# Kernel optimization log

Measured on AMD Instinct MI355X. Metric: run time of the kernel, lower is better.

## Reference

```python
import jax, jax.numpy as jnp
import numpy as np
from jax import lax

B, T = 512, 2048
VOCAB, E, H, OUT = 50257, 8, 2, 128


def _lstm_layer(x_seq, W_ih, W_hh, b):
    """x_seq: [B,T,D]; W_ih: [4H,D]; W_hh: [4H,H]; b: [4H] (b_ih+b_hh)."""
    Bn = x_seq.shape[0]
    gates_x = jnp.einsum('btd,gd->btg', x_seq, W_ih) + b  # [B,T,4H]
    h0 = jnp.zeros((Bn, H), x_seq.dtype)
    c0 = jnp.zeros((Bn, H), x_seq.dtype)

    def step(carry, gx):
        h, c = carry
        g = gx + h @ W_hh.T  # [B,4H]
        i, f, gg, o = jnp.split(g, 4, axis=-1)
        c = jax.nn.sigmoid(f) * c + jax.nn.sigmoid(i) * jnp.tanh(gg)
        h = jax.nn.sigmoid(o) * jnp.tanh(c)
        return (h, c), h

    (hT, cT), ys = lax.scan(step, (h0, c0), gates_x.transpose(1, 0, 2))
    return ys.transpose(1, 0, 2), hT, cT  # [B,T,H], [B,H], [B,H]


def setup_inputs() -> dict:
    key = jax.random.key(0)
    ks = jax.random.split(key, 10)
    s = lambda fan: 1.0 / np.sqrt(fan)
    u = lambda k, shape, a: jax.random.uniform(k, shape, jnp.float32, -a, a)
    x = jax.random.randint(ks[0], (B, T), 0, VOCAB)
    emb = jax.random.normal(ks[1], (VOCAB, E), jnp.float32)
    a = s(H)
    W_ih0 = u(ks[2], (4 * H, E), a)
    W_hh0 = u(ks[3], (4 * H, H), a)
    b0 = u(ks[4], (4 * H,), a) * 2.0  # b_ih + b_hh combined
    W_ih1 = u(ks[5], (4 * H, H), a)
    W_hh1 = u(ks[6], (4 * H, H), a)
    b1 = u(ks[7], (4 * H,), a) * 2.0
    W_fc = u(ks[8], (OUT, H), s(H))
    b_fc = u(ks[9], (OUT,), s(H))
    return {"x": x, "emb": emb, "W_ih0": W_ih0, "W_hh0": W_hh0, "b0": b0,
            "W_ih1": W_ih1, "W_hh1": W_hh1, "b1": b1, "W_fc": W_fc, "b_fc": b_fc}


def reference(x, emb, W_ih0, W_hh0, b0, W_ih1, W_hh1, b1, W_fc, b_fc):
    embedded = emb[x]  # [B,T,E]
    y0, h0, c0 = _lstm_layer(embedded, W_ih0, W_hh0, b0)
    y1, h1, c1 = _lstm_layer(y0, W_ih1, W_hh1, b1)
    h_n = jnp.stack([h0, h1], axis=0)  # [n_layer,B,H]
    c_n = jnp.stack([c0, c1], axis=0)
    out = y1.reshape(-1, H) @ W_fc.T + b_fc  # [B*T, OUT]
    return out, h_n, c_n
```

## Files before the change

kernel.cpp:

```cpp
#include <hip/hip_runtime.h>

#define VOCAB 50257
#define NB 512
#define NT 2048
#define NOUT 128
#define CHUNK 32
#define L2E 1.4426950408889634f

#define QP_XOR1 0xB1
#define QP_PAIR 0xA0
#define QP_CROSS 0x0A

template<int CTRL>
__device__ __forceinline__ float qp(float v){
    return __int_as_float(__builtin_amdgcn_update_dpp(0, __float_as_int(v), CTRL, 0xF, 0xF, true));
}

__global__ __launch_bounds__(256) void build_table(const float* __restrict__ emb,
                                                   const float* __restrict__ Wih0,
                                                   const float* __restrict__ b0,
                                                   float* __restrict__ tab){
    int v = blockIdx.x*256 + threadIdx.x;
    if (v >= VOCAB) return;
    const float4* ep = (const float4*)(emb + (size_t)v*8);
    float4 e0 = ep[0], e1 = ep[1];
    float e[8] = {e0.x,e0.y,e0.z,e0.w,e1.x,e1.y,e1.z,e1.w};
    const int perm[8] = {0,2,4,6,1,3,5,7};
    float o[8];
#pragma unroll
    for (int p=0;p<8;p++){
        int rj = perm[p];
        float s = b0[rj];
#pragma unroll
        for (int d=0;d<8;d++) s = fmaf(e[d], Wih0[rj*8+d], s);
        o[p] = s * ((rj==4||rj==5) ? 2.0f*L2E : -L2E);
    }
    float4* tp = (float4*)(tab + (size_t)v*8);
    tp[0] = make_float4(o[0],o[1],o[2],o[3]);
    tp[1] = make_float4(o[4],o[5],o[6],o[7]);
}

__global__ __launch_bounds__(256) void expand_gates(const int* __restrict__ x,
                                                    const float* __restrict__ tab,
                                                    float4* __restrict__ gx){
    int gid = blockIdx.x*256 + threadIdx.x;
    int t = gid >> 9;
    int b = gid & (NB-1);
    int tok = x[(size_t)b*NT + t];
    const float4* tp = (const float4*)tab + (size_t)tok*2;
    float4 v0 = tp[0], v1 = tp[1];
    gx[(size_t)gid*2]   = v0;
    gx[(size_t)gid*2+1] = v1;
}

#define GATE_COMBINE(x0, x1) { \
    float ex0 = __builtin_amdgcn_exp2f(x0); \
    float ex1 = __builtin_amdgcn_exp2f(x1); \
    float r0 = __builtin_amdgcn_rcpf(1.0f+ex0); \
    float r1 = __builtin_amdgcn_rcpf(1.0f+ex1); \
    float v0 = fmaf(B0, r0, A0); \
    float u0 = qp<QP_XOR1>(v0); \
    float u1 = qp<QP_XOR1>(r1); \
    c = fmaf(r1, c, v0*u0); \
    float e2c = __builtin_amdgcn_exp2f(2.0f*L2E*c); \
    float th = fmaf(-2.0f, __builtin_amdgcn_rcpf(1.0f+e2c), 1.0f); \
    float hh = u1*th; \
    hs = qp<QP_PAIR>(hh); \
    ho = qp<QP_CROSS>(hh); }

__global__ __launch_bounds__(128) void lstm_pipe(const float2* __restrict__ gx,
                                                 const float* __restrict__ Whh0,
                                                 const float* __restrict__ Wih1,
                                                 const float* __restrict__ Whh1,
                                                 const float* __restrict__ b1,
                                                 float* __restrict__ y1out,
                                                 float* __restrict__ tail){
    __shared__ float h0buf[2][CHUNK][16][2];
    const int tid  = threadIdx.x;
    const int wv   = tid >> 6;
    const int lane = tid & 63;
    const int l    = lane & 3;
    const int lrow = lane >> 2;
    const int row  = blockIdx.x*16 + lrow;
    const int e    = l >> 1;
    const int rj0  = (l&1)*4 + e;
    const int rj1  = rj0 + 2;
    const float s0 = (l&1) ? 2.0f*L2E : -L2E;
    const float s1 = -L2E;
    const float A0 = (l&1) ? 1.0f : 0.0f;
    const float B0 = (l&1) ? -2.0f : 1.0f;

    const float wS0 = Whh0[rj0*2+e]*s0,  wO0 = Whh0[rj0*2+(e^1)]*s0;
    const float wS1 = Whh0[rj1*2+e]*s1,  wO1 = Whh0[rj1*2+(e^1)]*s1;
    const float wi00 = Wih1[rj0*2+0]*s0, wi01 = Wih1[rj0*2+1]*s0;
    const float wi10 = Wih1[rj1*2+0]*s1, wi11 = Wih1[rj1*2+1]*s1;
    const float whS0 = Whh1[rj0*2+e]*s0, whO0 = Whh1[rj0*2+(e^1)]*s0;
    const float whS1 = Whh1[rj1*2+e]*s1, whO1 = Whh1[rj1*2+(e^1)]*s1;
    const float bb0  = b1[rj0]*s0,       bb1  = b1[rj1]*s1;

    float hs=0.f, ho=0.f, c=0.f;
    const size_t ST = (size_t)NB*4;
    const float2* __restrict__ gp = gx + (size_t)row*4 + l;
    float2 f0,f1,f2,f3,f4,f5,f6,f7;
    if (wv==0){
        f0=gp[0*ST]; f1=gp[1*ST]; f2=gp[2*ST]; f3=gp[3*ST];
        f4=gp[4*ST]; f5=gp[5*ST]; f6=gp[6*ST]; f7=gp[7*ST];
    }

    for (int cidx=0; cidx<=NT/CHUNK; ++cidx){
        if (wv==0){
            if (cidx < NT/CHUNK){
                const int buf = cidx & 1;
                const int base = cidx*CHUNK;
#define PSTEP(F, SS) { \
    float2 nf = gp[(size_t)(base+(SS)+8)*ST];  \
    float x0 = fmaf(wS0,hs, fmaf(wO0,ho, F.x)); \
    float x1 = fmaf(wS1,hs, fmaf(wO1,ho, F.y)); \
    GATE_COMBINE(x0, x1) \
    h0buf[buf][SS][lrow][e] = hs; \
    F = nf; }
                for (int s=0; s<CHUNK; s+=8){
                    PSTEP(f0,s+0) PSTEP(f1,s+1) PSTEP(f2,s+2) PSTEP(f3,s+3)
                    PSTEP(f4,s+4) PSTEP(f5,s+5) PSTEP(f6,s+6) PSTEP(f7,s+7)
                }
#undef PSTEP
            }
        } else {
            if (cidx >= 1){
                const int buf = (cidx-1) & 1;
                const int base = (cidx-1)*CHUNK;
#pragma unroll 8
                for (int s=0; s<CHUNK; ++s){
                    const float2 h0v = *(const float2*)&h0buf[buf][s][lrow][0];
                    float x0 = fmaf(whS0,hs, fmaf(whO0,ho, fmaf(wi00,h0v.x, fmaf(wi01,h0v.y, bb0))));
                    float x1 = fmaf(whS1,hs, fmaf(whO1,ho, fmaf(wi10,h0v.x, fmaf(wi11,h0v.y, bb1))));
                    GATE_COMBINE(x0, x1)
                    y1out[((size_t)(base+s)*NB + row)*2 + e] = hs;
                }
            }
        }
        __syncthreads();
    }
    const float cs = qp<QP_PAIR>(c);
    if (wv==0){
        tail[row*2+e]          = hs;
        tail[2*NB*2 + row*2+e] = cs;
    } else {
        tail[NB*2 + row*2+e]   = hs;
        tail[3*NB*2 + row*2+e] = cs;
    }
}

__global__ __launch_bounds__(256) void fc_out(const float* __restrict__ y1,
                                              const float* __restrict__ Wfc,
                                              const float* __restrict__ bfc,
                                              float* __restrict__ out){
    const int tid = threadIdx.x;
    const int j4  = tid & 31;
    const int btl = tid >> 5;
    const int bt  = blockIdx.x*8 + btl;
    const int b   = bt >> 11;
    const int tt  = bt & (NT-1);
    const float2 y  = *(const float2*)(y1 + ((size_t)tt*NB + b)*2);
    const float4 wa = *(const float4*)(Wfc + j4*8);
    const float4 wb = *(const float4*)(Wfc + j4*8+4);
    const float4 bbv= *(const float4*)(bfc + j4*4);
    float4 o;
    o.x = fmaf(y.x,wa.x, fmaf(y.y,wa.y, bbv.x));
    o.y = fmaf(y.x,wa.z, fmaf(y.y,wa.w, bbv.y));
    o.z = fmaf(y.x,wb.x, fmaf(y.y,wb.y, bbv.z));
    o.w = fmaf(y.x,wb.z, fmaf(y.y,wb.w, bbv.w));
    *(float4*)(out + (size_t)bt*128 + j4*4) = o;
}

extern "C" void kernel_launch(void* const* d_in, const int* in_sizes, int n_in,
                              void* d_out, int out_size, void* d_ws, size_t ws_size,
                              hipStream_t stream){
    const int*   x    = (const int*)d_in[0];
    const float* emb  = (const float*)d_in[1];
    const float* Wih0 = (const float*)d_in[2];
    const float* Whh0 = (const float*)d_in[3];
    const float* b0   = (const float*)d_in[4];
    const float* Wih1 = (const float*)d_in[5];
    const float* Whh1 = (const float*)d_in[6];
    const float* b1   = (const float*)d_in[7];
    const float* Wfc  = (const float*)d_in[8];
    const float* bfc  = (const float*)d_in[9];
    float* out  = (float*)d_out;
    float* tab  = (float*)d_ws;
    float* y1   = tab + (size_t)VOCAB*8;
    float* tail = out + (size_t)NB*NT*NOUT;
    float4* gxs = (float4*)d_out;

    build_table<<<(VOCAB+255)/256, 256, 0, stream>>>(emb, Wih0, b0, tab);
    expand_gates<<<(NB*NT)/256, 256, 0, stream>>>(x, tab, gxs);
    lstm_pipe<<<32, 128, 0, stream>>>((const float2*)gxs, Whh0, Wih1, Whh1, b1, y1, tail);
    fc_out<<<(NB*NT)/8, 256, 0, stream>>>(y1, Wfc, bfc, out);
}
```

Baseline: 297.3 us.

## Interleave two independent batch rows per lane in LSTM recurrence to hide latency

Each lane now carries two independent batch rows (A and B) through both LSTM layers, interleaving their dependent recurrence steps. The grid is halved to 16 blocks, so each wave has two chains to alternate between and can hide the serial exp/rcp/DPP latency. The cell state is also stored pre-scaled by 2*log2(e), which removes one multiply from the critical path and is undone only when the final c is written. The cost is half as many blocks, so fewer CUs are busy, plus extra register use and a shallower gate prefetch depth (4 steps instead of 8).

```diff
diff --git a/kernel.cpp b/kernel.cpp
--- a/kernel.cpp
+++ b/kernel.cpp
@@ -6,6 +6,7 @@
 #define NOUT 128
 #define CHUNK 32
 #define L2E 1.4426950408889634f
+#define INV2L2E 0.34657359027997264f
 
 #define QP_XOR1 0xB1
 #define QP_PAIR 0xA0
@@ -53,7 +54,7 @@
     gx[(size_t)gid*2+1] = v1;
 }
 
-#define GATE_COMBINE(x0, x1) { \
+#define GATE_COMBINE(x0, x1, CC, HS, HO) { \
     float ex0 = __builtin_amdgcn_exp2f(x0); \
     float ex1 = __builtin_amdgcn_exp2f(x1); \
     float r0 = __builtin_amdgcn_rcpf(1.0f+ex0); \
@@ -61,12 +62,12 @@
     float v0 = fmaf(B0, r0, A0); \
     float u0 = qp<QP_XOR1>(v0); \
     float u1 = qp<QP_XOR1>(r1); \
-    c = fmaf(r1, c, v0*u0); \
-    float e2c = __builtin_amdgcn_exp2f(2.0f*L2E*c); \
+    CC = fmaf(r1, CC, v0*u0); \
+    float e2c = __builtin_amdgcn_exp2f(CC); \
     float th = fmaf(-2.0f, __builtin_amdgcn_rcpf(1.0f+e2c), 1.0f); \
     float hh = u1*th; \
-    hs = qp<QP_PAIR>(hh); \
-    ho = qp<QP_CROSS>(hh); }
+    HS = qp<QP_PAIR>(hh); \
+    HO = qp<QP_CROSS>(hh); }
 
 __global__ __launch_bounds__(128) void lstm_pipe(const float2* __restrict__ gx,
                                                  const float* __restrict__ Whh0,
@@ -75,20 +76,21 @@
                                                  const float* __restrict__ b1,
                                                  float* __restrict__ y1out,
                                                  float* __restrict__ tail){
-    __shared__ float h0buf[2][CHUNK][16][2];
+    __shared__ float h0buf[2][CHUNK][32][2];
     const int tid  = threadIdx.x;
     const int wv   = tid >> 6;
     const int lane = tid & 63;
     const int l    = lane & 3;
-    const int lrow = lane >> 2;
-    const int row  = blockIdx.x*16 + lrow;
+    const int q    = lane >> 2;
+    const int rowA = blockIdx.x*32 + q;
+    const int rowB = rowA + 16;
     const int e    = l >> 1;
     const int rj0  = (l&1)*4 + e;
     const int rj1  = rj0 + 2;
     const float s0 = (l&1) ? 2.0f*L2E : -L2E;
     const float s1 = -L2E;
-    const float A0 = (l&1) ? 1.0f : 0.0f;
-    const float B0 = (l&1) ? -2.0f : 1.0f;
+    const float A0 = (l&1) ? 2.0f*L2E : 0.0f;
+    const float B0 = (l&1) ? -4.0f*L2E : 1.0f;
 
     const float wS0 = Whh0[rj0*2+e]*s0,  wO0 = Whh0[rj0*2+(e^1)]*s0;
     const float wS1 = Whh0[rj1*2+e]*s1,  wO1 = Whh0[rj1*2+(e^1)]*s1;
@@ -98,56 +100,71 @@
     const float whS1 = Whh1[rj1*2+e]*s1, whO1 = Whh1[rj1*2+(e^1)]*s1;
     const float bb0  = b1[rj0]*s0,       bb1  = b1[rj1]*s1;
 
-    float hs=0.f, ho=0.f, c=0.f;
+    float hsA=0.f, hoA=0.f, cA=0.f;
+    float hsB=0.f, hoB=0.f, cB=0.f;
     const size_t ST = (size_t)NB*4;
-    const float2* __restrict__ gp = gx + (size_t)row*4 + l;
-    float2 f0,f1,f2,f3,f4,f5,f6,f7;
+    const float2* __restrict__ gpA = gx + (size_t)rowA*4 + l;
+    const float2* __restrict__ gpB = gx + (size_t)rowB*4 + l;
+    float2 a0,a1,a2,a3, b0v,b1v,b2v,b3v;
     if (wv==0){
-        f0=gp[0*ST]; f1=gp[1*ST]; f2=gp[2*ST]; f3=gp[3*ST];
-        f4=gp[4*ST]; f5=gp[5*ST]; f6=gp[6*ST]; f7=gp[7*ST];
-    }
+        a0=gpA[0*ST]; a1=gpA[1*ST]; a2=gpA[2*ST]; a3=gpA[3*ST];
+        b0v=gpB[0*ST]; b1v=gpB[1*ST]; b2v=gpB[2*ST]; b3v=gpB[3*ST];
+    }
+
+#define PSTEP(F, GP, SS, BASE, BUF, CC, HS, HO, RQ) { \
+    float2 nf = GP[(size_t)((BASE)+(SS)+4)*ST];  \
+    float x0 = fmaf(wS0,HS, fmaf(wO0,HO, F.x)); \
+    float x1 = fmaf(wS1,HS, fmaf(wO1,HO, F.y)); \
+    GATE_COMBINE(x0, x1, CC, HS, HO) \
+    h0buf[BUF][SS][RQ][e] = HS; \
+    F = nf; }
+
+#define CSTEP(SS, BASE, BUF, CC, HS, HO, RQ, ROW) { \
+    const float2 h0v = *(const float2*)&h0buf[BUF][SS][RQ][0]; \
+    float x0 = fmaf(whS0,HS, fmaf(whO0,HO, fmaf(wi00,h0v.x, fmaf(wi01,h0v.y, bb0)))); \
+    float x1 = fmaf(whS1,HS, fmaf(whO1,HO, fmaf(wi10,h0v.x, fmaf(wi11,h0v.y, bb1)))); \
+    GATE_COMBINE(x0, x1, CC, HS, HO) \
+    y1out[((size_t)((BASE)+(SS))*NB + (ROW))*2 + e] = HS; }
 
     for (int cidx=0; cidx<=NT/CHUNK; ++cidx){
         if (wv==0){
             if (cidx < NT/CHUNK){
                 const int buf = cidx & 1;
                 const int base = cidx*CHUNK;
-#define PSTEP(F, SS) { \
-    float2 nf = gp[(size_t)(base+(SS)+8)*ST];  \
-    float x0 = fmaf(wS0,hs, fmaf(wO0,ho, F.x)); \
-    float x1 = fmaf(wS1,hs, fmaf(wO1,ho, F.y)); \
-    GATE_COMBINE(x0, x1) \
-    h0buf[buf][SS][lrow][e] = hs; \
-    F = nf; }
-                for (int s=0; s<CHUNK; s+=8){
-                    PSTEP(f0,s+0) PSTEP(f1,s+1) PSTEP(f2,s+2) PSTEP(f3,s+3)
-                    PSTEP(f4,s+4) PSTEP(f5,s+5) PSTEP(f6,s+6) PSTEP(f7,s+7)
+                for (int s=0; s<CHUNK; s+=4){
+                    PSTEP(a0, gpA, s+0, base, buf, cA, hsA, hoA, q)
+                    PSTEP(b0v, gpB, s+0, base, buf, cB, hsB, hoB, q+16)
+                    PSTEP(a1, gpA, s+1, base, buf, cA, hsA, hoA, q)
+                    PSTEP(b1v, gpB, s+1, base, buf, cB, hsB, hoB, q+16)
+                    PSTEP(a2, gpA, s+2, base, buf, cA, hsA, hoA, q)
+                    PSTEP(b2v, gpB, s+2, base, buf, cB, hsB, hoB, q+16)
+                    PSTEP(a3, gpA, s+3, base, buf, cA, hsA, hoA, q)
+                    PSTEP(b3v, gpB, s+3, base, buf, cB, hsB, hoB, q+16)
                 }
-#undef PSTEP
             }
         } else {
             if (cidx >= 1){
                 const int buf = (cidx-1) & 1;
                 const int base = (cidx-1)*CHUNK;
-#pragma unroll 8
+#pragma unroll 4
                 for (int s=0; s<CHUNK; ++s){
-                    const float2 h0v = *(const float2*)&h0buf[buf][s][lrow][0];
-                    float x0 = fmaf(whS0,hs, fmaf(whO0,ho, fmaf(wi00,h0v.x, fmaf(wi01,h0v.y, bb0))));
-                    float x1 = fmaf(whS1,hs, fmaf(whO1,ho, fmaf(wi10,h0v.x, fmaf(wi11,h0v.y, bb1))));
-                    GATE_COMBINE(x0, x1)
-                    y1out[((size_t)(base+s)*NB + row)*2 + e] = hs;
+                    CSTEP(s, base, buf, cA, hsA, hoA, q,    rowA)
+                    CSTEP(s, base, buf, cB, hsB, hoB, q+16, rowB)
                 }
             }
         }
         __syncthreads();
     }
-    const float cs = qp<QP_PAIR>(c);
+#undef PSTEP
+#undef CSTEP
+    const float csA = qp<QP_PAIR>(cA) * INV2L2E;
+    const float csB = qp<QP_PAIR>(cB) * INV2L2E;
     if (wv==0){
-        tail[row*2+e]          = hs;
-        tail[2*NB*2 + row*2+e] = cs;
+        tail[rowA*2+e]          = hsA;  tail[rowB*2+e]          = hsB;
+        tail[2*NB*2 + rowA*2+e] = csA;  tail[2*NB*2 + rowB*2+e] = csB;
     } else {
-        tail[NB*2 + row*2+e]   = hs;
-        tail[3*NB*2 + row*2+e] = cs;
+        tail[NB*2 + rowA*2+e]   = hsA;  tail[NB*2 + rowB*2+e]   = hsB;
+        tail[3*NB*2 + rowA*2+e] = csA;  tail[3*NB*2 + rowB*2+e] = csB;
     }
 }
 
@@ -194,6 +211,6 @@
 
     build_table<<<(VOCAB+255)/256, 256, 0, stream>>>(emb, Wih0, b0, tab);
     expand_gates<<<(NB*NT)/256, 256, 0, stream>>>(x, tab, gxs);
-    lstm_pipe<<<32, 128, 0, stream>>>((const float2*)gxs, Whh0, Wih1, Whh1, b1, y1, tail);
+    lstm_pipe<<<16, 128, 0, stream>>>((const float2*)gxs, Whh0, Wih1, Whh1, b1, y1, tail);
     fc_out<<<(NB*NT)/8, 256, 0, stream>>>(y1, Wfc, bfc, out);
 }
```

Result: slower. 415.2 us (+39.6%).

## Spread LSTM gates over 8 lanes per row and precompute layer-1 input

Applied to the files above, without the earlier changes.

Each batch row now uses 8 lanes, one gate per lane, instead of 4 lanes handling two gates each, so the grid doubles to 64 blocks. Gate values are combined through DPP broadcasts, and the cell state is kept pre-scaled by 2*log2(e) so the tanh needs no extra multiply. The layer-0 wave now computes layer 1's input projection itself and hands it through shared memory, which shortens layer 1's critical path. The cost is more DPP ops per step and twice the lanes per row.

```diff
diff --git a/kernel.cpp b/kernel.cpp
--- a/kernel.cpp
+++ b/kernel.cpp
@@ -6,14 +6,21 @@
 #define NOUT 128
 #define CHUNK 32
 #define L2E 1.4426950408889634f
-
-#define QP_XOR1 0xB1
-#define QP_PAIR 0xA0
-#define QP_CROSS 0x0A
+#define INV2L2E 0.34657359027997264f
+
+#define DPP_XOR1 0xB1
+#define DPP_B0   0x00
+#define DPP_B2   0xAA
+#define DPP_B3   0xFF
+#define DPP_HMIR 0x141
 
 template<int CTRL>
 __device__ __forceinline__ float qp(float v){
     return __int_as_float(__builtin_amdgcn_update_dpp(0, __float_as_int(v), CTRL, 0xF, 0xF, true));
+}
+
+__device__ __forceinline__ int gate_rj(int gi, int e){
+    return (gi==0) ? e : (gi==1) ? 4+e : (gi==2) ? 2+e : 6+e;
 }
 
 __global__ __launch_bounds__(256) void build_table(const float* __restrict__ emb,
@@ -25,15 +32,15 @@
     const float4* ep = (const float4*)(emb + (size_t)v*8);
     float4 e0 = ep[0], e1 = ep[1];
     float e[8] = {e0.x,e0.y,e0.z,e0.w,e1.x,e1.y,e1.z,e1.w};
-    const int perm[8] = {0,2,4,6,1,3,5,7};
     float o[8];
 #pragma unroll
-    for (int p=0;p<8;p++){
-        int rj = perm[p];
+    for (int l=0;l<8;l++){
+        int gi = l&3, el = l>>2;
+        int rj = gate_rj(gi, el);
         float s = b0[rj];
 #pragma unroll
         for (int d=0;d<8;d++) s = fmaf(e[d], Wih0[rj*8+d], s);
-        o[p] = s * ((rj==4||rj==5) ? 2.0f*L2E : -L2E);
+        o[l] = s * ((gi==1) ? 2.0f*L2E : -L2E);
     }
     float4* tp = (float4*)(tab + (size_t)v*8);
     tp[0] = make_float4(o[0],o[1],o[2],o[3]);
@@ -53,101 +60,105 @@
     gx[(size_t)gid*2+1] = v1;
 }
 
-#define GATE_COMBINE(x0, x1) { \
-    float ex0 = __builtin_amdgcn_exp2f(x0); \
-    float ex1 = __builtin_amdgcn_exp2f(x1); \
-    float r0 = __builtin_amdgcn_rcpf(1.0f+ex0); \
-    float r1 = __builtin_amdgcn_rcpf(1.0f+ex1); \
-    float v0 = fmaf(B0, r0, A0); \
-    float u0 = qp<QP_XOR1>(v0); \
-    float u1 = qp<QP_XOR1>(r1); \
-    c = fmaf(r1, c, v0*u0); \
-    float e2c = __builtin_amdgcn_exp2f(2.0f*L2E*c); \
-    float th = fmaf(-2.0f, __builtin_amdgcn_rcpf(1.0f+e2c), 1.0f); \
-    float hh = u1*th; \
-    hs = qp<QP_PAIR>(hh); \
-    ho = qp<QP_CROSS>(hh); }
-
-__global__ __launch_bounds__(128) void lstm_pipe(const float2* __restrict__ gx,
+#define GATE8(x, CC, HOwn, HOth) { \
+    float ex = __builtin_amdgcn_exp2f(x); \
+    float r  = __builtin_amdgcn_rcpf(1.0f+ex); \
+    float v  = fmaf(Bc, r, Ac); \
+    float u  = qp<DPP_XOR1>(v); \
+    float pr = v*u;                        \
+    float prb= qp<DPP_B0>(pr); \
+    float fv = qp<DPP_B2>(v); \
+    CC = fmaf(fv, CC, prb); \
+    float e2 = __builtin_amdgcn_exp2f(CC); \
+    float r2 = __builtin_amdgcn_rcpf(1.0f+e2); \
+    float th = fmaf(-2.0f, r2, 1.0f); \
+    float ov = qp<DPP_B3>(v); \
+    float hh = ov*th;                      \
+    HOwn = hh; \
+    HOth = qp<DPP_HMIR>(hh); }
+
+__global__ __launch_bounds__(128) void lstm_pipe(const float* __restrict__ gx,
                                                  const float* __restrict__ Whh0,
                                                  const float* __restrict__ Wih1,
                                                  const float* __restrict__ Whh1,
                                                  const float* __restrict__ b1,
                                                  float* __restrict__ y1out,
                                                  float* __restrict__ tail){
-    __shared__ float h0buf[2][CHUNK][16][2];
+    __shared__ float xpre[2][CHUNK][8][8];
     const int tid  = threadIdx.x;
     const int wv   = tid >> 6;
     const int lane = tid & 63;
-    const int l    = lane & 3;
-    const int lrow = lane >> 2;
-    const int row  = blockIdx.x*16 + lrow;
-    const int e    = l >> 1;
-    const int rj0  = (l&1)*4 + e;
-    const int rj1  = rj0 + 2;
-    const float s0 = (l&1) ? 2.0f*L2E : -L2E;
-    const float s1 = -L2E;
-    const float A0 = (l&1) ? 1.0f : 0.0f;
-    const float B0 = (l&1) ? -2.0f : 1.0f;
-
-    const float wS0 = Whh0[rj0*2+e]*s0,  wO0 = Whh0[rj0*2+(e^1)]*s0;
-    const float wS1 = Whh0[rj1*2+e]*s1,  wO1 = Whh0[rj1*2+(e^1)]*s1;
-    const float wi00 = Wih1[rj0*2+0]*s0, wi01 = Wih1[rj0*2+1]*s0;
-    const float wi10 = Wih1[rj1*2+0]*s1, wi11 = Wih1[rj1*2+1]*s1;
-    const float whS0 = Whh1[rj0*2+e]*s0, whO0 = Whh1[rj0*2+(e^1)]*s0;
-    const float whS1 = Whh1[rj1*2+e]*s1, whO1 = Whh1[rj1*2+(e^1)]*s1;
-    const float bb0  = b1[rj0]*s0,       bb1  = b1[rj1]*s1;
-
-    float hs=0.f, ho=0.f, c=0.f;
-    const size_t ST = (size_t)NB*4;
-    const float2* __restrict__ gp = gx + (size_t)row*4 + l;
-    float2 f0,f1,f2,f3,f4,f5,f6,f7;
-    if (wv==0){
-        f0=gp[0*ST]; f1=gp[1*ST]; f2=gp[2*ST]; f3=gp[3*ST];
-        f4=gp[4*ST]; f5=gp[5*ST]; f6=gp[6*ST]; f7=gp[7*ST];
-    }
+    const int l    = lane & 7;
+    const int q    = lane >> 3;
+    const int row  = blockIdx.x*8 + q;
+    const int gi   = l & 3;
+    const int e    = l >> 2;
+    const int rj   = gate_rj(gi, e);
+    const float s  = (gi==1) ? 2.0f*L2E : -L2E;
+    const float Ac = (gi==1) ? 2.0f*L2E : 0.0f;
+    const float Bc = (gi==1) ? -4.0f*L2E : 1.0f;
+
+    const float wOwn0 = Whh0[rj*2+e]*s,     wOth0 = Whh0[rj*2+(e^1)]*s;
+    const float wiOwn = Wih1[rj*2+e]*s,     wiOth = Wih1[rj*2+(e^1)]*s;
+    const float bb    = b1[rj]*s;
+    const float whOwn = Whh1[rj*2+e]*s,     whOth = Whh1[rj*2+(e^1)]*s;
+
+    float hOwn=0.f, hOth=0.f, c=0.f;
+    const size_t ST = (size_t)NB*8;
+    const float* __restrict__ gp = gx + (size_t)row*8 + l;
+    float a0=0.f,a1=0.f,a2=0.f,a3=0.f;
+    if (wv==0){ a0=gp[0*ST]; a1=gp[1*ST]; a2=gp[2*ST]; a3=gp[3*ST]; }
+    const bool st = (gi==0);
+
+#define PSTEP(F, SS, BASE, BUF) { \
+    float nf = gp[(size_t)((BASE)+(SS)+4)*ST];  \
+    float x = fmaf(wOwn0,hOwn, fmaf(wOth0,hOth, F)); \
+    GATE8(x, c, hOwn, hOth) \
+    float xp = fmaf(wiOwn,hOwn, fmaf(wiOth,hOth, bb)); \
+    xpre[BUF][SS][q][l] = xp; \
+    F = nf; }
+
+#define CSTEP(SS, BASE, BUF) { \
+    float xv = xpre[BUF][SS][q][l]; \
+    float x = fmaf(whOwn,hOwn, fmaf(whOth,hOth, xv)); \
+    GATE8(x, c, hOwn, hOth) \
+    if (st) y1out[((size_t)((BASE)+(SS))*NB + row)*2 + e] = hOwn; }
 
     for (int cidx=0; cidx<=NT/CHUNK; ++cidx){
         if (wv==0){
             if (cidx < NT/CHUNK){
                 const int buf = cidx & 1;
                 const int base = cidx*CHUNK;
-#define PSTEP(F, SS) { \
-    float2 nf = gp[(size_t)(base+(SS)+8)*ST];  \
-    float x0 = fmaf(wS0,hs, fmaf(wO0,ho, F.x)); \
-    float x1 = fmaf(wS1,hs, fmaf(wO1,ho, F.y)); \
-    GATE_COMBINE(x0, x1) \
-    h0buf[buf][SS][lrow][e] = hs; \
-    F = nf; }
-                for (int s=0; s<CHUNK; s+=8){
-                    PSTEP(f0,s+0) PSTEP(f1,s+1) PSTEP(f2,s+2) PSTEP(f3,s+3)
-                    PSTEP(f4,s+4) PSTEP(f5,s+5) PSTEP(f6,s+6) PSTEP(f7,s+7)
+                for (int ss=0; ss<CHUNK; ss+=4){
+                    PSTEP(a0, ss+0, base, buf)
+                    PSTEP(a1, ss+1, base, buf)
+                    PSTEP(a2, ss+2, base, buf)
+                    PSTEP(a3, ss+3, base, buf)
                 }
-#undef PSTEP
             }
         } else {
             if (cidx >= 1){
                 const int buf = (cidx-1) & 1;
                 const int base = (cidx-1)*CHUNK;
 #pragma unroll 8
-                for (int s=0; s<CHUNK; ++s){
-                    const float2 h0v = *(const float2*)&h0buf[buf][s][lrow][0];
-                    float x0 = fmaf(whS0,hs, fmaf(whO0,ho, fmaf(wi00,h0v.x, fmaf(wi01,h0v.y, bb0))));
-                    float x1 = fmaf(whS1,hs, fmaf(whO1,ho, fmaf(wi10,h0v.x, fmaf(wi11,h0v.y, bb1))));
-                    GATE_COMBINE(x0, x1)
-                    y1out[((size_t)(base+s)*NB + row)*2 + e] = hs;
+                for (int ss=0; ss<CHUNK; ++ss){
+                    CSTEP(ss, base, buf)
                 }
             }
         }
         __syncthreads();
     }
-    const float cs = qp<QP_PAIR>(c);
-    if (wv==0){
-        tail[row*2+e]          = hs;
-        tail[2*NB*2 + row*2+e] = cs;
-    } else {
-        tail[NB*2 + row*2+e]   = hs;
-        tail[3*NB*2 + row*2+e] = cs;
+#undef PSTEP
+#undef CSTEP
+    if (st){
+        const float cs = c * INV2L2E;
+        if (wv==0){
+            tail[row*2+e]          = hOwn;
+            tail[2*NB*2 + row*2+e] = cs;
+        } else {
+            tail[NB*2 + row*2+e]   = hOwn;
+            tail[3*NB*2 + row*2+e] = cs;
+        }
     }
 }
 
@@ -194,6 +205,6 @@
 
     build_table<<<(VOCAB+255)/256, 256, 0, stream>>>(emb, Wih0, b0, tab);
     expand_gates<<<(NB*NT)/256, 256, 0, stream>>>(x, tab, gxs);
-    lstm_pipe<<<32, 128, 0, stream>>>((const float2*)gxs, Whh0, Wih1, Whh1, b1, y1, tail);
+    lstm_pipe<<<64, 128, 0, stream>>>((const float*)gxs, Whh0, Wih1, Whh1, b1, y1, tail);
     fc_out<<<(NB*NT)/8, 256, 0, stream>>>(y1, Wfc, bfc, out);
 }
```

After: 341.6 us. 1.15x slower.

## Fuse gate expansion, LSTM scan and FC into one persistent flag-synchronized kernel

Applied to the files above, without the earlier changes.

Replaces the separate expand_gates, lstm_pipe and fc_out launches with one kernel. 32 blocks run the recurrent scan while 224 worker blocks expand gate inputs and then compute the FC output, coordinated through global atomic flags per 32-step chunk. This overlaps the memory-bound expansion and FC writes with the latency-bound serial scan. FC writes that would overwrite the gx buffer (which aliases the output) are deferred until all chunks finish. The cost is spin-wait polling, fewer prefetched gate values (4 instead of 8), and correctness depends on all blocks being co-resident.

```diff
diff --git a/kernel.cpp b/kernel.cpp
--- a/kernel.cpp
+++ b/kernel.cpp
@@ -5,6 +5,9 @@
 #define NT 2048
 #define NOUT 128
 #define CHUNK 32
+#define NCHUNK 64
+#define NSCAN 32
+#define NFC 224
 #define L2E 1.4426950408889634f
 
 #define QP_XOR1 0xB1
@@ -14,6 +17,10 @@
 template<int CTRL>
 __device__ __forceinline__ float qp(float v){
     return __int_as_float(__builtin_amdgcn_update_dpp(0, __float_as_int(v), CTRL, 0xF, 0xF, true));
+}
+
+__device__ __forceinline__ void spinwait(int* f, int target){
+    while (atomicAdd(f, 0) < target) __builtin_amdgcn_s_sleep(8);
 }
 
 __global__ __launch_bounds__(256) void build_table(const float* __restrict__ emb,
@@ -40,20 +47,7 @@
     tp[1] = make_float4(o[4],o[5],o[6],o[7]);
 }
 
-__global__ __launch_bounds__(256) void expand_gates(const int* __restrict__ x,
-                                                    const float* __restrict__ tab,
-                                                    float4* __restrict__ gx){
-    int gid = blockIdx.x*256 + threadIdx.x;
-    int t = gid >> 9;
-    int b = gid & (NB-1);
-    int tok = x[(size_t)b*NT + t];
-    const float4* tp = (const float4*)tab + (size_t)tok*2;
-    float4 v0 = tp[0], v1 = tp[1];
-    gx[(size_t)gid*2]   = v0;
-    gx[(size_t)gid*2+1] = v1;
-}
-
-#define GATE_COMBINE(x0, x1) { \
+#define GATE_COMBINE(x0, x1, CC, HS, HO) { \
     float ex0 = __builtin_amdgcn_exp2f(x0); \
     float ex1 = __builtin_amdgcn_exp2f(x1); \
     float r0 = __builtin_amdgcn_rcpf(1.0f+ex0); \
@@ -61,116 +55,161 @@
     float v0 = fmaf(B0, r0, A0); \
     float u0 = qp<QP_XOR1>(v0); \
     float u1 = qp<QP_XOR1>(r1); \
-    c = fmaf(r1, c, v0*u0); \
-    float e2c = __builtin_amdgcn_exp2f(2.0f*L2E*c); \
+    CC = fmaf(r1, CC, v0*u0); \
+    float e2c = __builtin_amdgcn_exp2f(2.0f*L2E*CC); \
     float th = fmaf(-2.0f, __builtin_amdgcn_rcpf(1.0f+e2c), 1.0f); \
     float hh = u1*th; \
-    hs = qp<QP_PAIR>(hh); \
-    ho = qp<QP_CROSS>(hh); }
-
-__global__ __launch_bounds__(128) void lstm_pipe(const float2* __restrict__ gx,
-                                                 const float* __restrict__ Whh0,
-                                                 const float* __restrict__ Wih1,
-                                                 const float* __restrict__ Whh1,
-                                                 const float* __restrict__ b1,
-                                                 float* __restrict__ y1out,
-                                                 float* __restrict__ tail){
+    HS = qp<QP_PAIR>(hh); \
+    HO = qp<QP_CROSS>(hh); }
+
+__global__ __launch_bounds__(128) void fused(const int* __restrict__ x,
+                                             const float* __restrict__ tab,
+                                             float* __restrict__ gx,
+                                             const float* __restrict__ Whh0,
+                                             const float* __restrict__ Wih1,
+                                             const float* __restrict__ Whh1,
+                                             const float* __restrict__ b1,
+                                             const float* __restrict__ Wfc,
+                                             const float* __restrict__ bfc,
+                                             float* __restrict__ y1out,
+                                             float* __restrict__ out,
+                                             float* __restrict__ tail,
+                                             int* __restrict__ ef,
+                                             int* __restrict__ sf){
     __shared__ float h0buf[2][CHUNK][16][2];
-    const int tid  = threadIdx.x;
-    const int wv   = tid >> 6;
-    const int lane = tid & 63;
-    const int l    = lane & 3;
-    const int lrow = lane >> 2;
-    const int row  = blockIdx.x*16 + lrow;
-    const int e    = l >> 1;
-    const int rj0  = (l&1)*4 + e;
-    const int rj1  = rj0 + 2;
-    const float s0 = (l&1) ? 2.0f*L2E : -L2E;
-    const float s1 = -L2E;
-    const float A0 = (l&1) ? 1.0f : 0.0f;
-    const float B0 = (l&1) ? -2.0f : 1.0f;
-
-    const float wS0 = Whh0[rj0*2+e]*s0,  wO0 = Whh0[rj0*2+(e^1)]*s0;
-    const float wS1 = Whh0[rj1*2+e]*s1,  wO1 = Whh0[rj1*2+(e^1)]*s1;
-    const float wi00 = Wih1[rj0*2+0]*s0, wi01 = Wih1[rj0*2+1]*s0;
-    const float wi10 = Wih1[rj1*2+0]*s1, wi11 = Wih1[rj1*2+1]*s1;
-    const float whS0 = Whh1[rj0*2+e]*s0, whO0 = Whh1[rj0*2+(e^1)]*s0;
-    const float whS1 = Whh1[rj1*2+e]*s1, whO1 = Whh1[rj1*2+(e^1)]*s1;
-    const float bb0  = b1[rj0]*s0,       bb1  = b1[rj1]*s1;
-
-    float hs=0.f, ho=0.f, c=0.f;
-    const size_t ST = (size_t)NB*4;
-    const float2* __restrict__ gp = gx + (size_t)row*4 + l;
-    float2 f0,f1,f2,f3,f4,f5,f6,f7;
-    if (wv==0){
-        f0=gp[0*ST]; f1=gp[1*ST]; f2=gp[2*ST]; f3=gp[3*ST];
-        f4=gp[4*ST]; f5=gp[5*ST]; f6=gp[6*ST]; f7=gp[7*ST];
-    }
-
-    for (int cidx=0; cidx<=NT/CHUNK; ++cidx){
-        if (wv==0){
-            if (cidx < NT/CHUNK){
-                const int buf = cidx & 1;
-                const int base = cidx*CHUNK;
-#define PSTEP(F, SS) { \
-    float2 nf = gp[(size_t)(base+(SS)+8)*ST];  \
-    float x0 = fmaf(wS0,hs, fmaf(wO0,ho, F.x)); \
-    float x1 = fmaf(wS1,hs, fmaf(wO1,ho, F.y)); \
-    GATE_COMBINE(x0, x1) \
-    h0buf[buf][SS][lrow][e] = hs; \
+    const int tid = threadIdx.x;
+
+    if (blockIdx.x < NSCAN){
+        const int wv   = tid >> 6;
+        const int lane = tid & 63;
+        const int l    = lane & 3;
+        const int lrow = lane >> 2;
+        const int row  = blockIdx.x*16 + lrow;
+        const int e    = l >> 1;
+        const int rj0  = (l&1)*4 + e;
+        const int rj1  = rj0 + 2;
+        const float s0 = (l&1) ? 2.0f*L2E : -L2E;
+        const float s1 = -L2E;
+        const float A0 = (l&1) ? 1.0f : 0.0f;
+        const float B0 = (l&1) ? -2.0f : 1.0f;
+
+        const float wS0 = Whh0[rj0*2+e]*s0,  wO0 = Whh0[rj0*2+(e^1)]*s0;
+        const float wS1 = Whh0[rj1*2+e]*s1,  wO1 = Whh0[rj1*2+(e^1)]*s1;
+        const float wi00 = Wih1[rj0*2+0]*s0, wi01 = Wih1[rj0*2+1]*s0;
+        const float wi10 = Wih1[rj1*2+0]*s1, wi11 = Wih1[rj1*2+1]*s1;
+        const float whS0 = Whh1[rj0*2+e]*s0, whO0 = Whh1[rj0*2+(e^1)]*s0;
+        const float whS1 = Whh1[rj1*2+e]*s1, whO1 = Whh1[rj1*2+(e^1)]*s1;
+        const float bb0  = b1[rj0]*s0,       bb1  = b1[rj1]*s1;
+
+        float hsA=0.f, hoA=0.f, cA=0.f;
+        const size_t ST = (size_t)NB*4;
+        const float2* __restrict__ gp = (const float2*)gx + (size_t)row*4 + l;
+
+        if (tid==0){ spinwait(ef+0, 32); spinwait(ef+1, 32); }
+        __syncthreads();
+        __threadfence();
+
+        float2 a0,a1,a2,a3;
+        a0=make_float2(0,0);a1=a0;a2=a0;a3=a0;
+        if (wv==0){ a0=gp[0*ST]; a1=gp[1*ST]; a2=gp[2*ST]; a3=gp[3*ST]; }
+
+#define PSTEP(F, SS, BASE, BUF) { \
+    float2 nf = gp[(size_t)((BASE)+(SS)+4)*ST]; \
+    float x0 = fmaf(wS0,hsA, fmaf(wO0,hoA, F.x)); \
+    float x1 = fmaf(wS1,hsA, fmaf(wO1,hoA, F.y)); \
+    GATE_COMBINE(x0, x1, cA, hsA, hoA) \
+    h0buf[BUF][SS][lrow][e] = hsA; \
     F = nf; }
-                for (int s=0; s<CHUNK; s+=8){
-                    PSTEP(f0,s+0) PSTEP(f1,s+1) PSTEP(f2,s+2) PSTEP(f3,s+3)
-                    PSTEP(f4,s+4) PSTEP(f5,s+5) PSTEP(f6,s+6) PSTEP(f7,s+7)
+
+#define CSTEP(SS, BASE, BUF) { \
+    const float2 h0v = *(const float2*)&h0buf[BUF][SS][lrow][0]; \
+    float x0 = fmaf(whS0,hsA, fmaf(whO0,hoA, fmaf(wi00,h0v.x, fmaf(wi01,h0v.y, bb0)))); \
+    float x1 = fmaf(whS1,hsA, fmaf(whO1,hoA, fmaf(wi10,h0v.x, fmaf(wi11,h0v.y, bb1)))); \
+    GATE_COMBINE(x0, x1, cA, hsA, hoA) \
+    y1out[((size_t)((BASE)+(SS))*NB + row)*2 + e] = hsA; }
+
+        for (int cidx=0; cidx<=NCHUNK; ++cidx){
+            if (tid==0 && cidx+1 < NCHUNK) spinwait(ef+cidx+1, 32);
+            __syncthreads();
+            if (wv==0){
+                if (cidx < NCHUNK){
+                    const int buf = cidx & 1;
+                    const int base = cidx*CHUNK;
+                    for (int ss=0; ss<CHUNK; ss+=4){
+                        PSTEP(a0, ss+0, base, buf)
+                        PSTEP(a1, ss+1, base, buf)
+                        PSTEP(a2, ss+2, base, buf)
+                        PSTEP(a3, ss+3, base, buf)
+                    }
                 }
-#undef PSTEP
-            }
-        } else {
-            if (cidx >= 1){
-                const int buf = (cidx-1) & 1;
-                const int base = (cidx-1)*CHUNK;
-#pragma unroll 8
-                for (int s=0; s<CHUNK; ++s){
-                    const float2 h0v = *(const float2*)&h0buf[buf][s][lrow][0];
-                    float x0 = fmaf(whS0,hs, fmaf(whO0,ho, fmaf(wi00,h0v.x, fmaf(wi01,h0v.y, bb0))));
-                    float x1 = fmaf(whS1,hs, fmaf(whO1,ho, fmaf(wi10,h0v.x, fmaf(wi11,h0v.y, bb1))));
-                    GATE_COMBINE(x0, x1)
-                    y1out[((size_t)(base+s)*NB + row)*2 + e] = hs;
+            } else {
+                if (cidx >= 1){
+                    const int buf = (cidx-1) & 1;
+                    const int base = (cidx-1)*CHUNK;
+#pragma unroll 4
+                    for (int ss=0; ss<CHUNK; ++ss){
+                        CSTEP(ss, base, buf)
+                    }
                 }
             }
-        }
-        __syncthreads();
+            __syncthreads();
+            if (tid==0 && cidx>=1){ __threadfence(); atomicAdd(&sf[cidx-1], 1); }
+        }
+#undef PSTEP
+#undef CSTEP
+        const float cs = qp<QP_PAIR>(cA);
+        if (wv==0){
+            tail[row*2+e]          = hsA;
+            tail[2*NB*2 + row*2+e] = cs;
+        } else {
+            tail[NB*2 + row*2+e]   = hsA;
+            tail[3*NB*2 + row*2+e] = cs;
+        }
+    } else {
+        const int i = blockIdx.x - NSCAN;
+        for (int t = i; t < NT; t += NFC){
+#pragma unroll
+            for (int p=0;p<4;p++){
+                int b = tid + p*128;
+                int tok = x[(size_t)b*NT + t];
+                const float4* tp = (const float4*)tab + (size_t)tok*2;
+                float4 v0 = tp[0], v1 = tp[1];
+                float4* gp4 = (float4*)gx + ((size_t)t*NB + b)*2;
+                gp4[0] = v0; gp4[1] = v1;
+            }
+            __syncthreads();
+            if (tid==0){ __threadfence(); atomicAdd(&ef[t>>5], 1); }
+        }
+        const int j4 = tid & 31, g = tid >> 5;
+        const float4 wa  = ((const float4*)Wfc)[j4*2];
+        const float4 wb  = ((const float4*)Wfc)[j4*2+1];
+        const float4 bbv = ((const float4*)bfc)[j4];
+#define FCWRITE(T, B) { \
+    const float2 y = *(const float2*)(y1out + ((size_t)(T)*NB + (B))*2); \
+    float4 o; \
+    o.x = fmaf(y.x,wa.x, fmaf(y.y,wa.y, bbv.x)); \
+    o.y = fmaf(y.x,wa.z, fmaf(y.y,wa.w, bbv.y)); \
+    o.z = fmaf(y.x,wb.x, fmaf(y.y,wb.y, bbv.z)); \
+    o.w = fmaf(y.x,wb.z, fmaf(y.y,wb.w, bbv.w)); \
+    *(float4*)(out + ((size_t)(B)*NT + (T))*128 + j4*4) = o; }
+        for (int c=0; c<NCHUNK; ++c){
+            if (tid==0) spinwait(&sf[c], NSCAN);
+            __syncthreads();
+            __threadfence();
+            for (int base = i*4; base < 480*CHUNK; base += NFC*4){
+                int ll = base + g;
+                int t = c*CHUNK + (ll & 31);
+                int b = 32 + (ll >> 5);
+                FCWRITE(t, b)
+            }
+        }
+        for (int base = i*4; base < 32*NT; base += NFC*4){
+            int ll = base + g;
+            int b = ll >> 11, t = ll & (NT-1);
+            FCWRITE(t, b)
+        }
+#undef FCWRITE
     }
-    const float cs = qp<QP_PAIR>(c);
-    if (wv==0){
-        tail[row*2+e]          = hs;
-        tail[2*NB*2 + row*2+e] = cs;
-    } else {
-        tail[NB*2 + row*2+e]   = hs;
-        tail[3*NB*2 + row*2+e] = cs;
-    }
-}
-
-__global__ __launch_bounds__(256) void fc_out(const float* __restrict__ y1,
-                                              const float* __restrict__ Wfc,
-                                              const float* __restrict__ bfc,
-                                              float* __restrict__ out){
-    const int tid = threadIdx.x;
-    const int j4  = tid & 31;
-    const int btl = tid >> 5;
-    const int bt  = blockIdx.x*8 + btl;
-    const int b   = bt >> 11;
-    const int tt  = bt & (NT-1);
-    const float2 y  = *(const float2*)(y1 + ((size_t)tt*NB + b)*2);
-    const float4 wa = *(const float4*)(Wfc + j4*8);
-    const float4 wb = *(const float4*)(Wfc + j4*8+4);
-    const float4 bbv= *(const float4*)(bfc + j4*4);
-    float4 o;
-    o.x = fmaf(y.x,wa.x, fmaf(y.y,wa.y, bbv.x));
-    o.y = fmaf(y.x,wa.z, fmaf(y.y,wa.w, bbv.y));
-    o.z = fmaf(y.x,wb.x, fmaf(y.y,wb.y, bbv.z));
-    o.w = fmaf(y.x,wb.z, fmaf(y.y,wb.w, bbv.w));
-    *(float4*)(out + (size_t)bt*128 + j4*4) = o;
 }
 
 extern "C" void kernel_launch(void* const* d_in, const int* in_sizes, int n_in,
@@ -189,11 +228,13 @@
     float* out  = (float*)d_out;
     float* tab  = (float*)d_ws;
     float* y1   = tab + (size_t)VOCAB*8;
+    int*   ef   = (int*)(y1 + (size_t)NT*NB*2);
+    int*   sf   = ef + 64;
     float* tail = out + (size_t)NB*NT*NOUT;
-    float4* gxs = (float4*)d_out;
-
+    float* gxs  = out;
+
+    hipMemsetAsync(ef, 0, 128*sizeof(int), stream);
     build_table<<<(VOCAB+255)/256, 256, 0, stream>>>(emb, Wih0, b0, tab);
-    expand_gates<<<(NB*NT)/256, 256, 0, stream>>>(x, tab, gxs);
-    lstm_pipe<<<32, 128, 0, stream>>>((const float2*)gxs, Whh0, Wih1, Whh1, b1, y1, tail);
-    fc_out<<<(NB*NT)/8, 256, 0, stream>>>(y1, Wfc, bfc, out);
-}
+    fused<<<NSCAN+NFC, 128, 0, stream>>>(x, tab, gxs, Whh0, Wih1, Whh1, b1,
+                                         Wfc, bfc, y1, out, tail, ef, sf);
+}
```

Measured after the change: 1.099 ms. 270% more time.
